# Optimization experiments

Measured on AMD Instinct MI355X. Metric: run time of the kernel, lower is better.

The kernel has to match this reference:

```python
import jax, jax.numpy as jnp
import numpy as np

B, S, D, E, K = 4, 4096, 2048, 64, 2
H = D // 2  # router hidden dim
LN_EPS = 1e-5


def setup_inputs() -> dict:
    key = jax.random.key(0)
    kx, k1, k2 = jax.random.split(key, 3)
    # Xavier-uniform-ish scales for the two linears
    s1 = float(np.sqrt(6.0 / (D + H)))
    s2 = float(np.sqrt(6.0 / (H + E)))
    return {
        "x": jax.random.normal(kx, (B, S, D), dtype=jnp.float32),
        "W1": jax.random.uniform(k1, (D, H), jnp.float32, -s1, s1),
        "b1": jnp.zeros((H,), jnp.float32),
        "gamma": jnp.ones((H,), jnp.float32),
        "beta": jnp.zeros((H,), jnp.float32),
        "W2": jax.random.uniform(k2, (H, E), jnp.float32, -s2, s2),
        "b2": jnp.zeros((E,), jnp.float32),
    }


def reference(x, W1, b1, gamma, beta, W2, b2):
    # x: [B,S,D] -> flatten tokens
    xf = x.reshape(-1, D)                       # [N, D]
    h = xf @ W1 + b1                            # [N, H]
    mu = jnp.mean(h, axis=-1, keepdims=True)
    var = jnp.var(h, axis=-1, keepdims=True)
    h = (h - mu) * jax.lax.rsqrt(var + LN_EPS) * gamma + beta
    h = jax.nn.gelu(h, approximate=False)       # torch nn.GELU default = exact erf
    logits = h @ W2 + b2                        # [N, E]
    probs = jax.nn.softmax(logits, axis=-1)
    w, idx = jax.lax.top_k(probs, K)            # [N, K]
    w = w / (jnp.sum(w, axis=-1, keepdims=True) + 1e-9)
    idx = idx.reshape(B, S, K)
    w = w.reshape(B, S, K)
    return idx, w, logits
```

## Files before the change

kernel.cpp:

```cpp
#include <hip/hip_runtime.h>
#include <hip/hip_bf16.h>
#include <cmath>

#define N_TOK 16384
#define D_DIM 2048
#define H_DIM 1024
#define E_DIM 64

typedef _Float16 half8 __attribute__((ext_vector_type(8)));
typedef float floatx4 __attribute__((ext_vector_type(4)));

#define GLOAD_LDS(gp, lp)                                                      \
  __builtin_amdgcn_global_load_lds(                                            \
      (const __attribute__((address_space(1))) unsigned int*)(gp),             \
      (__attribute__((address_space(3))) unsigned int*)(lp), 16, 0, 0)

__global__ __launch_bounds__(256) void splitT_w1_kernel(
    const float* __restrict__ W1, _Float16* __restrict__ whT,
    _Float16* __restrict__ wlT) {
  __shared__ float ls[64][65];
  const int k0 = blockIdx.x * 64;
  const int c0 = blockIdx.y * 64;
  const int t = threadIdx.x;
  const int tr = t >> 6;
  const int tc = t & 63;
#pragma unroll
  for (int i = 0; i < 16; i++) {
    int k = tr * 16 + i;
    ls[k][tc] = W1[(size_t)(k0 + k) * H_DIM + c0 + tc];
  }
  __syncthreads();
#pragma unroll
  for (int i = 0; i < 16; i++) {
    int c = tr * 16 + i;
    float v = ls[tc][c];
    _Float16 hv = (_Float16)v;
    _Float16 lv = (_Float16)(v - (float)hv);
    whT[(size_t)(c0 + c) * D_DIM + k0 + tc] = hv;
    wlT[(size_t)(c0 + c) * D_DIM + k0 + tc] = lv;
  }
}

__global__ __launch_bounds__(256) void pack_w2_kernel(
    const float* __restrict__ W2, _Float16* __restrict__ pW2h,
    _Float16* __restrict__ pW2l) {
  const int s = blockIdx.x;
  const int ng = threadIdx.x >> 6;
  const int lane = threadIdx.x & 63;
  const int kg = lane >> 4, fr = lane & 15;
  half8 hh, ll;
#pragma unroll
  for (int j = 0; j < 8; j++) {
    const float v = W2[(size_t)(s * 32 + kg * 8 + j) * E_DIM + ng * 16 + fr];
    const _Float16 hv = (_Float16)v;
    hh[j] = hv;
    ll[j] = (_Float16)(v - (float)hv);
  }
  const size_t idx = (((size_t)s * 4 + ng) * 64 + lane) * 8;
  *(half8*)(pW2h + idx) = hh;
  *(half8*)(pW2l + idx) = ll;
}

__global__ __launch_bounds__(1024, 4) void gemm1_mfma_kernel(
    const float* __restrict__ x, const _Float16* __restrict__ whT,
    const _Float16* __restrict__ wlT, float* __restrict__ h) {
  extern __shared__ __align__(16) char smem[];

  const int t = threadIdx.x;
  const int wave = t >> 6;
  const int lane = t & 63;

  const int bid = blockIdx.x;
  const int swz = (bid & 7) * 32 + (bid >> 3);
  const int by = swz >> 2, bx = swz & 3;
  const int row0 = by * 256, col0 = bx * 256;
  const int wr = wave >> 2, wc = wave & 3;

  floatx4 acc[4][4];
#pragma unroll
  for (int m = 0; m < 4; m++)
#pragma unroll
    for (int n = 0; n < 4; n++) acc[m][n] = (floatx4){0.f, 0.f, 0.f, 0.f};

  const int arow = t >> 2;
  const int aslot = t & 3;
  const int awaddr = arow * 64 + ((aslot ^ ((arow >> 1) & 3)) << 4);
  const size_t gaoff = (size_t)(row0 + arow) * D_DIM + aslot * 8;

  const int bo_ = t * 16;
  const int brow = bo_ >> 6;
  const int bss = ((bo_ >> 4) & 3) ^ ((brow >> 1) & 3);
  const int ldsBoff = wave * 1024;
  const size_t gboff = (size_t)(col0 + brow) * D_DIM + bss * 8;

  const int kg = lane >> 4;
  const int fr = lane & 15;

  int afr[4], bfr[4];
#pragma unroll
  for (int m = 0; m < 4; m++) {
    const int r = wr * 64 + m * 16 + fr;
    afr[m] = r * 64 + ((kg ^ ((r >> 1) & 3)) << 4);
  }
#pragma unroll
  for (int n = 0; n < 4; n++) {
    const int c = wc * 64 + n * 16 + fr;
    bfr[n] = c * 64 + ((kg ^ ((c >> 1) & 3)) << 4);
  }

  float4 av0, av1;

#define LOAD_A(T)                                                              \
  do {                                                                         \
    const float* pa = x + gaoff + (size_t)(T) * 32;                            \
    av0 = *(const float4*)pa;                                                  \
    av1 = *(const float4*)(pa + 4);                                            \
  } while (0)

#define WRITE_A(B)                                                             \
  do {                                                                         \
    char* lb = smem + (B) * 65536;                                             \
    float vs[8] = {av0.x, av0.y, av0.z, av0.w, av1.x, av1.y, av1.z, av1.w};    \
    half8 hh, ll;                                                              \
    _Pragma("unroll") for (int j = 0; j < 8; j++) {                            \
      _Float16 hv = (_Float16)vs[j];                                           \
      hh[j] = hv;                                                              \
      ll[j] = (_Float16)(vs[j] - (float)hv);                                   \
    }                                                                          \
    *(half8*)(lb + awaddr) = hh;                                               \
    *(half8*)(lb + 16384 + awaddr) = ll;                                       \
  } while (0)

#define GLD_B(T)                                                               \
  do {                                                                         \
    const size_t kk = (size_t)(T) * 32;                                        \
    char* db = smem + ((T) & 1) * 65536;                                       \
    GLOAD_LDS(whT + gboff + kk, db + 32768 + ldsBoff);                         \
    GLOAD_LDS(wlT + gboff + kk, db + 49152 + ldsBoff);                         \
  } while (0)

#define BODY(T, STG)                                                           \
  do {                                                                         \
    const char* cb = smem + ((T) & 1) * 65536;                                 \
    if ((STG) < 2) GLD_B((T) + 1);                                             \
    __builtin_amdgcn_sched_barrier(0);                                         \
    half8 bh[4], bl[4];                                                        \
    _Pragma("unroll") for (int n = 0; n < 4; n++) {                            \
      bh[n] = *(const half8*)(cb + 32768 + bfr[n]);                            \
      bl[n] = *(const half8*)(cb + 49152 + bfr[n]);                            \
    }                                                                          \
    _Pragma("unroll") for (int m = 0; m < 4; m++) {                            \
      half8 ah = *(const half8*)(cb + afr[m]);                                 \
      half8 al = *(const half8*)(cb + 16384 + afr[m]);                         \
      __builtin_amdgcn_s_setprio(1);                                           \
      _Pragma("unroll") for (int n = 0; n < 4; n++) {                          \
        acc[m][n] = __builtin_amdgcn_mfma_f32_16x16x32_f16(ah, bh[n],          \
                                                           acc[m][n], 0, 0, 0);\
        acc[m][n] = __builtin_amdgcn_mfma_f32_16x16x32_f16(ah, bl[n],          \
                                                           acc[m][n], 0, 0, 0);\
        acc[m][n] = __builtin_amdgcn_mfma_f32_16x16x32_f16(al, bh[n],          \
                                                           acc[m][n], 0, 0, 0);\
      }                                                                        \
      __builtin_amdgcn_s_setprio(0);                                           \
    }                                                                          \
    __builtin_amdgcn_sched_barrier(0);                                         \
    if ((STG) < 2) {                                                           \
      WRITE_A(((T) + 1) & 1);                                                  \
      if ((STG) == 0) {                                                        \
        LOAD_A((T) + 2);                                                       \
        __builtin_amdgcn_sched_barrier(0);                                     \
        asm volatile("s_waitcnt vmcnt(2)" ::: "memory");                       \
      } else {                                                                 \
        __builtin_amdgcn_sched_barrier(0);                                     \
        asm volatile("s_waitcnt vmcnt(0)" ::: "memory");                       \
      }                                                                        \
      asm volatile("s_waitcnt lgkmcnt(0)" ::: "memory");                       \
      __builtin_amdgcn_s_barrier();                                            \
      __builtin_amdgcn_sched_barrier(0);                                       \
    }                                                                          \
  } while (0)

  LOAD_A(0);
  GLD_B(0);
  WRITE_A(0);
  LOAD_A(1);
  asm volatile("s_waitcnt vmcnt(2)" ::: "memory");
  asm volatile("s_waitcnt lgkmcnt(0)" ::: "memory");
  __builtin_amdgcn_s_barrier();
  __builtin_amdgcn_sched_barrier(0);

#pragma unroll 1
  for (int T = 0; T < 62; ++T) {
    BODY(T, 0);
  }
  BODY(62, 1);
  BODY(63, 2);

#undef LOAD_A
#undef WRITE_A
#undef GLD_B
#undef BODY

  const int rj = (lane >> 4) * 4;
#pragma unroll
  for (int m = 0; m < 4; m++) {
    const int rbase = row0 + wr * 64 + m * 16 + rj;
#pragma unroll
    for (int n = 0; n < 4; n++) {
      const int c = col0 + wc * 64 + n * 16 + fr;
#pragma unroll
      for (int j = 0; j < 4; j++) {
        h[(size_t)(rbase + j) * H_DIM + c] = acc[m][n][j];
      }
    }
  }
}

__device__ __forceinline__ float gelu_exact(float v) {
  return 0.5f * v * (1.0f + erff(v * 0.70710678118654752f));
}

__global__ __launch_bounds__(256) void router_kernel(
    const float* __restrict__ hbuf, const float* __restrict__ b1,
    const float* __restrict__ gamma, const float* __restrict__ beta,
    const _Float16* __restrict__ pW2h, const _Float16* __restrict__ pW2l,
    const float* __restrict__ b2, float* __restrict__ out) {
  extern __shared__ __align__(16) char rsm[];
  char* gh = rsm;
  char* gl = rsm + 16384;
  float* lg = (float*)(rsm + 32768);

  const int t = threadIdx.x;
  const int tok0 = blockIdx.x * 8;

  const int tk = t >> 5;
  const int l32 = t & 31;
  {
    const float* hr = hbuf + (size_t)(tok0 + tk) * H_DIM;
    float vals[32];
    float s = 0.f, s2 = 0.f;
#pragma unroll
    for (int q = 0; q < 4; q++) {
      const int j = q * 256 + l32 * 8;
      float4 v0 = *(const float4*)(hr + j);
      float4 v1 = *(const float4*)(hr + j + 4);
      float4 b0 = *(const float4*)(b1 + j);
      float4 b1v = *(const float4*)(b1 + j + 4);
      v0.x += b0.x; v0.y += b0.y; v0.z += b0.z; v0.w += b0.w;
      v1.x += b1v.x; v1.y += b1v.y; v1.z += b1v.z; v1.w += b1v.w;
      vals[q * 8 + 0] = v0.x; vals[q * 8 + 1] = v0.y;
      vals[q * 8 + 2] = v0.z; vals[q * 8 + 3] = v0.w;
      vals[q * 8 + 4] = v1.x; vals[q * 8 + 5] = v1.y;
      vals[q * 8 + 6] = v1.z; vals[q * 8 + 7] = v1.w;
      s += v0.x + v0.y + v0.z + v0.w + v1.x + v1.y + v1.z + v1.w;
      s2 += v0.x * v0.x + v0.y * v0.y + v0.z * v0.z + v0.w * v0.w +
            v1.x * v1.x + v1.y * v1.y + v1.z * v1.z + v1.w * v1.w;
    }
#pragma unroll
    for (int off = 16; off; off >>= 1) {
      s += __shfl_xor(s, off, 32);
      s2 += __shfl_xor(s2, off, 32);
    }
    const float mean = s * (1.f / 1024.f);
    const float var = s2 * (1.f / 1024.f) - mean * mean;
    const float rstd = rsqrtf(var + 1e-5f);
    const int swz = (tk >> 1) & 3;
#pragma unroll
    for (int q = 0; q < 4; q++) {
      const int j = q * 256 + l32 * 8;
      float4 gm0 = *(const float4*)(gamma + j);
      float4 gm1 = *(const float4*)(gamma + j + 4);
      float4 bt0 = *(const float4*)(beta + j);
      float4 bt1 = *(const float4*)(beta + j + 4);
      float gms[8] = {gm0.x, gm0.y, gm0.z, gm0.w, gm1.x, gm1.y, gm1.z, gm1.w};
      float bts[8] = {bt0.x, bt0.y, bt0.z, bt0.w, bt1.x, bt1.y, bt1.z, bt1.w};
      half8 hh, ll;
#pragma unroll
      for (int e = 0; e < 8; e++) {
        const float gv =
            gelu_exact((vals[q * 8 + e] - mean) * rstd * gms[e] + bts[e]);
        const _Float16 hv = (_Float16)gv;
        hh[e] = hv;
        ll[e] = (_Float16)(gv - (float)hv);
      }
      const int sidx = q * 8 + (l32 >> 2);
      const int addr = sidx * 512 + tk * 64 + (((l32 & 3) ^ swz) << 4);
      *(half8*)(gh + addr) = hh;
      *(half8*)(gl + addr) = ll;
    }
  }
  __syncthreads();

  const int wave = t >> 6;
  const int lane = t & 63;
  const int kg = lane >> 4;
  const int fr = lane & 15;
  {
    floatx4 acc = (floatx4){0.f, 0.f, 0.f, 0.f};
    const int aswz = (fr >> 1) & 3;
#pragma unroll
    for (int s = 0; s < 32; s++) {
      const int aaddr = s * 512 + fr * 64 + ((kg ^ aswz) << 4);
      half8 ah = *(const half8*)(gh + aaddr);
      half8 al = *(const half8*)(gl + aaddr);
      const size_t bo = (((size_t)s * 4 + wave) * 64 + lane) * 8;
      half8 bh = *(const half8*)(pW2h + bo);
      half8 bl = *(const half8*)(pW2l + bo);
      acc = __builtin_amdgcn_mfma_f32_16x16x32_f16(ah, bh, acc, 0, 0, 0);
      acc = __builtin_amdgcn_mfma_f32_16x16x32_f16(ah, bl, acc, 0, 0, 0);
      acc = __builtin_amdgcn_mfma_f32_16x16x32_f16(al, bh, acc, 0, 0, 0);
    }
    if (kg < 2) {
#pragma unroll
      for (int j = 0; j < 4; j++) {
        lg[(kg * 4 + j) * E_DIM + wave * 16 + fr] = acc[j];
      }
    }
  }
  __syncthreads();

  float* out_idx = out;
  float* out_w = out + 32768;
  float* out_logits = out + 65536;

  const float b2v = b2[lane];
#pragma unroll
  for (int tt = 0; tt < 2; tt++) {
    const int tok = wave * 2 + tt;
    const int n = tok0 + tok;
    const float L = lg[tok * E_DIM + lane] + b2v;
    float m = L;
#pragma unroll
    for (int off = 32; off; off >>= 1) m = fmaxf(m, __shfl_xor(m, off));
    const float ex = expf(L - m);
    float sum = ex;
#pragma unroll
    for (int off = 32; off; off >>= 1) sum += __shfl_xor(sum, off);

    float v1 = L; int i1 = lane;
#pragma unroll
    for (int off = 32; off; off >>= 1) {
      float ov = __shfl_xor(v1, off);
      int oi = __shfl_xor(i1, off);
      if (ov > v1 || (ov == v1 && oi < i1)) { v1 = ov; i1 = oi; }
    }
    float v2 = (lane == i1) ? -1e30f : L; int i2 = lane;
#pragma unroll
    for (int off = 32; off; off >>= 1) {
      float ov = __shfl_xor(v2, off);
      int oi = __shfl_xor(i2, off);
      if (ov > v2 || (ov == v2 && oi < i2)) { v2 = ov; i2 = oi; }
    }

    out_logits[(size_t)n * 64 + lane] = L;
    if (lane == 0) {
      const float p1 = expf(v1 - m) / sum;
      const float p2 = expf(v2 - m) / sum;
      const float dn = p1 + p2 + 1e-9f;
      out_idx[n * 2 + 0] = (float)i1;
      out_idx[n * 2 + 1] = (float)i2;
      out_w[n * 2 + 0] = p1 / dn;
      out_w[n * 2 + 1] = p2 / dn;
    }
  }
}

extern "C" void kernel_launch(void* const* d_in, const int* in_sizes, int n_in,
                              void* d_out, int out_size, void* d_ws, size_t ws_size,
                              hipStream_t stream) {
  const float* x = (const float*)d_in[0];
  const float* W1 = (const float*)d_in[1];
  const float* b1 = (const float*)d_in[2];
  const float* gamma = (const float*)d_in[3];
  const float* beta = (const float*)d_in[4];
  const float* W2 = (const float*)d_in[5];
  const float* b2 = (const float*)d_in[6];
  float* out = (float*)d_out;

  char* ws = (char*)d_ws;
  _Float16* whT = (_Float16*)ws;
  _Float16* wlT = (_Float16*)(ws + 4194304);
  float* hbuf = (float*)(ws + 8388608);
  _Float16* pW2h = (_Float16*)(ws + 75497472);
  _Float16* pW2l = (_Float16*)(ws + 75628544);

  (void)hipFuncSetAttribute((const void*)gemm1_mfma_kernel,
                            hipFuncAttributeMaxDynamicSharedMemorySize,
                            131072);
  (void)hipFuncSetAttribute((const void*)router_kernel,
                            hipFuncAttributeMaxDynamicSharedMemorySize,
                            34816);

  splitT_w1_kernel<<<dim3(D_DIM / 64, H_DIM / 64), 256, 0, stream>>>(W1, whT, wlT);
  pack_w2_kernel<<<32, 256, 0, stream>>>(W2, pW2h, pW2l);

  gemm1_mfma_kernel<<<256, 1024, 131072, stream>>>(x, whT, wlT, hbuf);

  router_kernel<<<N_TOK / 8, 256, 34816, stream>>>(hbuf, b1, gamma, beta,
                                                   pW2h, pW2l, b2, out);
}
```

Baseline: 219.4 us.

## Merge weight-prep kernels, reorder GEMM inner MFMA loop, swizzle router token mapping

Combines the W1 split/transpose and W2 packing kernels into a single launch to remove one kernel launch. Restructures the GEMM inner loop to load B fragments two at a time, interleaving them with the A fragments, which lowers live register pressure for the B operands at the cost of reloading A fragments twice. Remaps router block indices so that consecutive blocks touch tokens spread across XCD-sized chunks, aiming for better L2 locality on hbuf reads.

```diff
diff --git a/kernel.cpp b/kernel.cpp
--- a/kernel.cpp
+++ b/kernel.cpp
@@ -15,50 +15,50 @@
       (const __attribute__((address_space(1))) unsigned int*)(gp),             \
       (__attribute__((address_space(3))) unsigned int*)(lp), 16, 0, 0)
 
-__global__ __launch_bounds__(256) void splitT_w1_kernel(
+__global__ __launch_bounds__(256) void prep_kernel(
     const float* __restrict__ W1, _Float16* __restrict__ whT,
-    _Float16* __restrict__ wlT) {
-  __shared__ float ls[64][65];
-  const int k0 = blockIdx.x * 64;
-  const int c0 = blockIdx.y * 64;
+    _Float16* __restrict__ wlT, const float* __restrict__ W2,
+    _Float16* __restrict__ pW2h, _Float16* __restrict__ pW2l) {
+  const int bid = blockIdx.x;
   const int t = threadIdx.x;
-  const int tr = t >> 6;
-  const int tc = t & 63;
-#pragma unroll
-  for (int i = 0; i < 16; i++) {
-    int k = tr * 16 + i;
-    ls[k][tc] = W1[(size_t)(k0 + k) * H_DIM + c0 + tc];
-  }
-  __syncthreads();
-#pragma unroll
-  for (int i = 0; i < 16; i++) {
-    int c = tr * 16 + i;
-    float v = ls[tc][c];
-    _Float16 hv = (_Float16)v;
-    _Float16 lv = (_Float16)(v - (float)hv);
-    whT[(size_t)(c0 + c) * D_DIM + k0 + tc] = hv;
-    wlT[(size_t)(c0 + c) * D_DIM + k0 + tc] = lv;
-  }
-}
-
-__global__ __launch_bounds__(256) void pack_w2_kernel(
-    const float* __restrict__ W2, _Float16* __restrict__ pW2h,
-    _Float16* __restrict__ pW2l) {
-  const int s = blockIdx.x;
-  const int ng = threadIdx.x >> 6;
-  const int lane = threadIdx.x & 63;
-  const int kg = lane >> 4, fr = lane & 15;
-  half8 hh, ll;
-#pragma unroll
-  for (int j = 0; j < 8; j++) {
-    const float v = W2[(size_t)(s * 32 + kg * 8 + j) * E_DIM + ng * 16 + fr];
-    const _Float16 hv = (_Float16)v;
-    hh[j] = hv;
-    ll[j] = (_Float16)(v - (float)hv);
-  }
-  const size_t idx = (((size_t)s * 4 + ng) * 64 + lane) * 8;
-  *(half8*)(pW2h + idx) = hh;
-  *(half8*)(pW2l + idx) = ll;
+  if (bid < 512) {
+    __shared__ float ls[64][65];
+    const int k0 = (bid & 31) * 64;
+    const int c0 = (bid >> 5) * 64;
+    const int tr = t >> 6;
+    const int tc = t & 63;
+#pragma unroll
+    for (int i = 0; i < 16; i++) {
+      int k = tr * 16 + i;
+      ls[k][tc] = W1[(size_t)(k0 + k) * H_DIM + c0 + tc];
+    }
+    __syncthreads();
+#pragma unroll
+    for (int i = 0; i < 16; i++) {
+      int c = tr * 16 + i;
+      float v = ls[tc][c];
+      _Float16 hv = (_Float16)v;
+      _Float16 lv = (_Float16)(v - (float)hv);
+      whT[(size_t)(c0 + c) * D_DIM + k0 + tc] = hv;
+      wlT[(size_t)(c0 + c) * D_DIM + k0 + tc] = lv;
+    }
+  } else {
+    const int s = bid - 512;
+    const int ng = t >> 6;
+    const int lane = t & 63;
+    const int kg = lane >> 4, fr = lane & 15;
+    half8 hh, ll;
+#pragma unroll
+    for (int j = 0; j < 8; j++) {
+      const float v = W2[(size_t)(s * 32 + kg * 8 + j) * E_DIM + ng * 16 + fr];
+      const _Float16 hv = (_Float16)v;
+      hh[j] = hv;
+      ll[j] = (_Float16)(v - (float)hv);
+    }
+    const size_t idx = (((size_t)s * 4 + ng) * 64 + lane) * 8;
+    *(half8*)(pW2h + idx) = hh;
+    *(half8*)(pW2l + idx) = ll;
+  }
 }
 
 __global__ __launch_bounds__(1024, 4) void gemm1_mfma_kernel(
@@ -144,24 +144,29 @@
     const char* cb = smem + ((T) & 1) * 65536;                                 \
     if ((STG) < 2) GLD_B((T) + 1);                                             \
     __builtin_amdgcn_sched_barrier(0);                                         \
-    half8 bh[4], bl[4];                                                        \
-    _Pragma("unroll") for (int n = 0; n < 4; n++) {                            \
-      bh[n] = *(const half8*)(cb + 32768 + bfr[n]);                            \
-      bl[n] = *(const half8*)(cb + 49152 + bfr[n]);                            \
-    }                                                                          \
-    _Pragma("unroll") for (int m = 0; m < 4; m++) {                            \
-      half8 ah = *(const half8*)(cb + afr[m]);                                 \
-      half8 al = *(const half8*)(cb + 16384 + afr[m]);                         \
-      __builtin_amdgcn_s_setprio(1);                                           \
-      _Pragma("unroll") for (int n = 0; n < 4; n++) {                          \
-        acc[m][n] = __builtin_amdgcn_mfma_f32_16x16x32_f16(ah, bh[n],          \
-                                                           acc[m][n], 0, 0, 0);\
-        acc[m][n] = __builtin_amdgcn_mfma_f32_16x16x32_f16(ah, bl[n],          \
-                                                           acc[m][n], 0, 0, 0);\
-        acc[m][n] = __builtin_amdgcn_mfma_f32_16x16x32_f16(al, bh[n],          \
-                                                           acc[m][n], 0, 0, 0);\
+    _Pragma("unroll") for (int np = 0; np < 2; np++) {                         \
+      half8 bh0 = *(const half8*)(cb + 32768 + bfr[2 * np]);                   \
+      half8 bl0 = *(const half8*)(cb + 49152 + bfr[2 * np]);                   \
+      half8 bh1 = *(const half8*)(cb + 32768 + bfr[2 * np + 1]);               \
+      half8 bl1 = *(const half8*)(cb + 49152 + bfr[2 * np + 1]);               \
+      _Pragma("unroll") for (int m = 0; m < 4; m++) {                          \
+        half8 ah = *(const half8*)(cb + afr[m]);                               \
+        half8 al = *(const half8*)(cb + 16384 + afr[m]);                       \
+        __builtin_amdgcn_s_setprio(1);                                         \
+        acc[m][2 * np] = __builtin_amdgcn_mfma_f32_16x16x32_f16(               \
+            ah, bh0, acc[m][2 * np], 0, 0, 0);                                 \
+        acc[m][2 * np] = __builtin_amdgcn_mfma_f32_16x16x32_f16(               \
+            ah, bl0, acc[m][2 * np], 0, 0, 0);                                 \
+        acc[m][2 * np] = __builtin_amdgcn_mfma_f32_16x16x32_f16(               \
+            al, bh0, acc[m][2 * np], 0, 0, 0);                                 \
+        acc[m][2 * np + 1] = __builtin_amdgcn_mfma_f32_16x16x32_f16(           \
+            ah, bh1, acc[m][2 * np + 1], 0, 0, 0);                             \
+        acc[m][2 * np + 1] = __builtin_amdgcn_mfma_f32_16x16x32_f16(           \
+            ah, bl1, acc[m][2 * np + 1], 0, 0, 0);                             \
+        acc[m][2 * np + 1] = __builtin_amdgcn_mfma_f32_16x16x32_f16(           \
+            al, bh1, acc[m][2 * np + 1], 0, 0, 0);                             \
+        __builtin_amdgcn_s_setprio(0);                                         \
       }                                                                        \
-      __builtin_amdgcn_s_setprio(0);                                           \
     }                                                                          \
     __builtin_amdgcn_sched_barrier(0);                                         \
     if ((STG) < 2) {                                                           \
@@ -231,7 +236,8 @@
   float* lg = (float*)(rsm + 32768);
 
   const int t = threadIdx.x;
-  const int tok0 = blockIdx.x * 8;
+  const int bid = blockIdx.x;
+  const int tok0 = (bid & 7) * 2048 + (bid >> 3) * 8;
 
   const int tk = t >> 5;
   const int l32 = t & 31;
@@ -391,8 +397,7 @@
                             hipFuncAttributeMaxDynamicSharedMemorySize,
                             34816);
 
-  splitT_w1_kernel<<<dim3(D_DIM / 64, H_DIM / 64), 256, 0, stream>>>(W1, whT, wlT);
-  pack_w2_kernel<<<32, 256, 0, stream>>>(W2, pW2h, pW2l);
+  prep_kernel<<<544, 256, 0, stream>>>(W1, whT, wlT, W2, pW2h, pW2l);
 
   gemm1_mfma_kernel<<<256, 1024, 131072, stream>>>(x, whT, wlT, hbuf);
 
```

Result: no change. 221.7 us (+1.0%).
